# Performance work log

Hardware: AMD Instinct MI355X
Metric: run time of the kernel (lower is better)

## Reference

```python
import jax, jax.numpy as jnp
import numpy as np

NUM_EXPERTS = 32
TOP_K = 8
HIDDEN = 1536
INTER = 512


def setup_inputs() -> dict:
    key = jax.random.key(0)
    k1, k2, k3, k4 = jax.random.split(key, 4)
    hidden_states = jax.random.normal(k1, (4, 2048, HIDDEN), dtype=jnp.float32)
    # gate (router) weight: [E, H] as in nn.Linear(hidden, num_experts)
    gate_w = jax.random.normal(k2, (NUM_EXPERTS, HIDDEN), dtype=jnp.float32) * 0.02
    # fused gate+up projection per expert: [E, 2*I, H] (first I rows = gate/silu path)
    w13 = jax.random.normal(k3, (NUM_EXPERTS, 2 * INTER, HIDDEN), dtype=jnp.float32) * 0.02
    # down projection per expert: [E, H, I]
    w2 = jax.random.normal(k4, (NUM_EXPERTS, HIDDEN, INTER), dtype=jnp.float32) * 0.02
    return {"hidden_states": hidden_states, "gate_w": gate_w, "w13": w13, "w2": w2}


def _moe_forward(x, gate_w, w13, w2):
    orig_shape = x.shape
    x = x.reshape(-1, HIDDEN)            # [T, H]
    T = x.shape[0]

    # Router: softmax over all experts, then top-k, then renormalize.
    router_logits = x @ gate_w.T          # [T, E]
    probs = jax.nn.softmax(router_logits, axis=-1)
    topk_w, topk_idx = jax.lax.top_k(probs, TOP_K)        # [T, K]
    topk_w = topk_w / jnp.sum(topk_w, axis=-1, keepdims=True)

    # Scatter top-k weights into a dense [T, E] combine matrix (zeros elsewhere).
    expert_w = jnp.zeros((T, NUM_EXPERTS), dtype=x.dtype)
    expert_w = expert_w.at[jnp.arange(T)[:, None], topk_idx].add(topk_w)
    expert_w_eT = expert_w.T              # [E, T]

    def body(acc, ew):
        we, w13_e, w2_e = ew              # [T], [2I, H], [H, I]
        gu = x @ w13_e.T                  # [T, 2I]
        g, u = gu[:, :INTER], gu[:, INTER:]
        y = (jax.nn.silu(g) * u) @ w2_e.T  # [T, H]
        return acc + we[:, None] * y, None

    out, _ = jax.lax.scan(body, jnp.zeros_like(x), (expert_w_eT, w13, w2))
    return out.reshape(orig_shape)


def reference(hidden_states, gate_w, w13, w2):
    return _moe_forward(hidden_states, gate_w, w13, w2)
```

## Files before the change

### kernel.cpp

```cpp
#include <hip/hip_runtime.h>
#include <hip/hip_bf16.h>
#include <math.h>

#define NUM_EXPERTS 32
#define TOP_K 8
#define HIDDEN 1536
#define INTER 512

typedef __bf16 bf16_t;
typedef __bf16 bf16x8 __attribute__((ext_vector_type(8)));
typedef __bf16 bf16x4 __attribute__((ext_vector_type(4)));
typedef float f32x4 __attribute__((ext_vector_type(4)));

#define M_COUNTS    0
#define M_OFFSETS   32
#define M_CURSORS   96
#define M_NUMTILES  128
#define M_TILE_E    256
#define M_TILE_M0   1024
#define M_TILE_ROWS 2048
#define META_BYTES  16384

__device__ __forceinline__ void gld16(void* lds, const void* gsrc) {
  __builtin_amdgcn_global_load_lds(
      (const __attribute__((address_space(1))) void*)gsrc,
      (__attribute__((address_space(3))) void*)lds, 16, 0, 0);
}

__global__ __launch_bounds__(256) void k_cvt(
    const float* __restrict__ src, bf16_t* __restrict__ dst)
{
  size_t i = ((size_t)blockIdx.x * 256 + threadIdx.x) * 4;
  f32x4 v = *(const f32x4*)(src + i);
  bf16x4 o;
  o[0] = (bf16_t)v[0]; o[1] = (bf16_t)v[1]; o[2] = (bf16_t)v[2]; o[3] = (bf16_t)v[3];
  *(bf16x4*)(dst + i) = o;
}

__global__ __launch_bounds__(256) void k_tgw(
    const float* __restrict__ gw, float* __restrict__ gwT4)
{
  int tid = blockIdx.x * 256 + threadIdx.x;
  int e = tid / HIDDEN, k = tid % HIDDEN;
  gwT4[(k >> 2) * 128 + (e << 2) + (k & 3)] = gw[tid];
}

__global__ __launch_bounds__(64) void k_router(
    const float* __restrict__ x, const float* __restrict__ gwT4,
    int* __restrict__ meta, int* __restrict__ topk_idx, float* __restrict__ topk_w,
    bf16_t* __restrict__ x16)
{
  int t = blockIdx.x;
  int lane = threadIdx.x;
  int e = lane & 31, part = lane >> 5;
  const float* xrow = x + (size_t)t * HIDDEN;
  const f32x4* xr = (const f32x4*)(xrow + part * 768);
  const f32x4* gr = (const f32x4*)(gwT4 + part * 192 * 128 + e * 4);
  float s = 0.f;
#pragma unroll 4
  for (int i = 0; i < 192; ++i) {
    f32x4 xv = xr[i];
    f32x4 gv = gr[i * 32];
    s += xv[0] * gv[0] + xv[1] * gv[1] + xv[2] * gv[2] + xv[3] * gv[3];
  }
  s += __shfl_xor(s, 32);

  {
    const f32x4* xv4 = (const f32x4*)(xrow + lane * 24);
    bf16_t* xo = x16 + (size_t)t * HIDDEN + lane * 24;
#pragma unroll
    for (int i = 0; i < 6; ++i) {
      f32x4 v = xv4[i];
      bf16x4 o;
      o[0] = (bf16_t)v[0]; o[1] = (bf16_t)v[1]; o[2] = (bf16_t)v[2]; o[3] = (bf16_t)v[3];
      *(bf16x4*)(xo + i * 4) = o;
    }
  }

  float logit = s, rem = s;
  float m0 = 0.f, wsum = 0.f, my_l = 0.f;
  int my_e = 0;
#pragma unroll
  for (int k = 0; k < TOP_K; ++k) {
    float mx = rem;
#pragma unroll
    for (int off = 32; off >= 1; off >>= 1) mx = fmaxf(mx, __shfl_xor(mx, off));
    unsigned long long bal = __ballot(rem == mx);
    int src = __ffsll(bal) - 1;
    int ex = src & 31;
    float lv = __shfl(logit, ex);
    if (k == 0) m0 = mx;
    wsum += __expf(lv - m0);
    if (lane == k) { my_e = ex; my_l = lv; }
    if ((lane & 31) == ex) rem = -1e30f;
  }
  if (lane < TOP_K) {
    topk_idx[t * TOP_K + lane] = my_e;
    topk_w[t * TOP_K + lane] = __expf(my_l - m0) / wsum;
    atomicAdd(&meta[M_COUNTS + my_e], 1);
  }
}

__global__ void k_scan(int* __restrict__ meta)
{
  if (threadIdx.x != 0 || blockIdx.x != 0) return;
  int off = 0, nt = 0;
  for (int e = 0; e < NUM_EXPERTS; ++e) {
    int n = meta[M_COUNTS + e];
    meta[M_OFFSETS + e] = off;
    meta[M_CURSORS + e] = off;
    int tn = (n + 127) >> 7;
    for (int i = 0; i < tn; ++i) {
      meta[M_TILE_E + nt] = e;
      meta[M_TILE_M0 + nt] = off + i * 128;
      meta[M_TILE_ROWS + nt] = min(128, n - i * 128);
      ++nt;
    }
    off += n;
  }
  meta[M_OFFSETS + NUM_EXPERTS] = off;
  meta[M_NUMTILES] = nt;
}

__global__ __launch_bounds__(256) void k_scatter(
    const int* __restrict__ topk_idx,
    int* __restrict__ meta, int* __restrict__ pair_token, int* __restrict__ pair_pos)
{
  int i = blockIdx.x * 256 + threadIdx.x;
  int e = topk_idx[i];
  int pos = atomicAdd(&meta[M_CURSORS + e], 1);
  pair_token[pos] = i >> 3;
  pair_pos[i] = pos;
}

__global__ __launch_bounds__(256, 3) void k_gemm1(
    const bf16_t* __restrict__ x, const bf16_t* __restrict__ w13,
    const int* __restrict__ meta, const int* __restrict__ pair_token,
    bf16_t* __restrict__ act)
{
  int bid = blockIdx.x;
  int xcd = bid & 7, r2 = bid >> 3;
  int nb = r2 & 3, tile = xcd + 8 * (r2 >> 2);
  if (tile >= meta[M_NUMTILES]) return;
  int e    = meta[M_TILE_E + tile];
  int m0   = meta[M_TILE_M0 + tile];
  int rows = meta[M_TILE_ROWS + tile];
  int n0g  = nb * 128;

  __shared__ __align__(16) char smem[49152];
  char* As = smem;
  char* Bs = smem + 16384;

  int tid = threadIdx.x;
  int lane = tid & 63, w = tid >> 6;
  int cd = lane & 7;
  int lrow = w * 8 + (lane >> 3);

  const bf16_t* a_src[4];
  const bf16_t* b_src[8];
#pragma unroll
  for (int i = 0; i < 4; ++i) {
    int r = i * 32 + lrow;
    int rr = (r < rows) ? r : 0;
    int tok = pair_token[m0 + rr];
    int cg = cd ^ (r & 7);
    a_src[i] = x + (size_t)tok * HIDDEN + cg * 8;
  }
#pragma unroll
  for (int i = 0; i < 8; ++i) {
    int r = i * 32 + lrow;
    int cg = cd ^ (r & 7);
    int gr = (r < 128) ? (n0g + r) : (512 + n0g + (r - 128));
    b_src[i] = w13 + (size_t)e * (2 * INTER) * HIDDEN + (size_t)gr * HIDDEN + cg * 8;
  }
  unsigned lds_off = w * 1024 + lane * 16;

  f32x4 acc[2][16] = {};
  int q = lane >> 4, cl = lane & 15;
  int arow0 = (w * 32 + cl) * 128;
  int arow1 = (w * 32 + 16 + cl) * 128;

  for (int k0 = 0; k0 < HIDDEN; k0 += 64) {
#pragma unroll
    for (int i = 0; i < 4; ++i) gld16(As + i * 4096 + lds_off, a_src[i] + k0);
#pragma unroll
    for (int i = 0; i < 8; ++i) gld16(Bs + i * 4096 + lds_off, b_src[i] + k0);
    __syncthreads();
#pragma unroll
    for (int ks = 0; ks < 2; ++ks) {
      int csw = ((ks * 4 + q) ^ (lane & 7)) * 16;
      bf16x8 a0 = *(const bf16x8*)(As + arow0 + csw);
      bf16x8 a1 = *(const bf16x8*)(As + arow1 + csw);
#pragma unroll
      for (int in = 0; in < 16; ++in) {
        bf16x8 b = *(const bf16x8*)(Bs + (in * 16 + cl) * 128 + csw);
        acc[0][in] = __builtin_amdgcn_mfma_f32_16x16x32_bf16(a0, b, acc[0][in], 0, 0, 0);
        acc[1][in] = __builtin_amdgcn_mfma_f32_16x16x32_bf16(a1, b, acc[1][in], 0, 0, 0);
      }
    }
    __syncthreads();
  }

#pragma unroll
  for (int im = 0; im < 2; ++im) {
#pragma unroll
    for (int reg = 0; reg < 4; ++reg) {
      int row = w * 32 + im * 16 + q * 4 + reg;
      if (row < rows) {
        bf16_t* obase = act + (size_t)(m0 + row) * INTER + n0g + cl;
#pragma unroll
        for (int in = 0; in < 8; ++in) {
          float g = acc[im][in][reg];
          float u = acc[im][in + 8][reg];
          float a = (g / (1.f + __expf(-g))) * u;
          obase[in * 16] = (bf16_t)a;
        }
      }
    }
  }
}

__global__ __launch_bounds__(256, 3) void k_gemm2(
    const bf16_t* __restrict__ act, const bf16_t* __restrict__ w2,
    const int* __restrict__ meta, bf16_t* __restrict__ y, int n0base)
{
  int bid = blockIdx.x;
  int xcd = bid & 7, r2 = bid >> 3;
  int nb = r2 % 3, tile = xcd + 8 * (r2 / 3);
  if (tile >= meta[M_NUMTILES]) return;
  int e    = meta[M_TILE_E + tile];
  int m0   = meta[M_TILE_M0 + tile];
  int rows = meta[M_TILE_ROWS + tile];
  int n0l  = nb * 256;
  int n0   = n0base + n0l;

  __shared__ __align__(16) char smem[49152];
  char* As = smem;
  char* Bs = smem + 16384;

  int tid = threadIdx.x;
  int lane = tid & 63, w = tid >> 6;
  int cd = lane & 7;
  int lrow = w * 8 + (lane >> 3);

  const bf16_t* a_src[4];
  const bf16_t* b_src[8];
#pragma unroll
  for (int i = 0; i < 4; ++i) {
    int r = i * 32 + lrow;
    int rr = (r < rows) ? r : 0;
    int cg = cd ^ (r & 7);
    a_src[i] = act + (size_t)(m0 + rr) * INTER + cg * 8;
  }
#pragma unroll
  for (int i = 0; i < 8; ++i) {
    int r = i * 32 + lrow;
    int cg = cd ^ (r & 7);
    b_src[i] = w2 + (size_t)e * HIDDEN * INTER + (size_t)(n0 + r) * INTER + cg * 8;
  }
  unsigned lds_off = w * 1024 + lane * 16;

  f32x4 acc[2][16] = {};
  int q = lane >> 4, cl = lane & 15;
  int arow0 = (w * 32 + cl) * 128;
  int arow1 = (w * 32 + 16 + cl) * 128;

  for (int k0 = 0; k0 < INTER; k0 += 64) {
#pragma unroll
    for (int i = 0; i < 4; ++i) gld16(As + i * 4096 + lds_off, a_src[i] + k0);
#pragma unroll
    for (int i = 0; i < 8; ++i) gld16(Bs + i * 4096 + lds_off, b_src[i] + k0);
    __syncthreads();
#pragma unroll
    for (int ks = 0; ks < 2; ++ks) {
      int csw = ((ks * 4 + q) ^ (lane & 7)) * 16;
      bf16x8 a0 = *(const bf16x8*)(As + arow0 + csw);
      bf16x8 a1 = *(const bf16x8*)(As + arow1 + csw);
#pragma unroll
      for (int in = 0; in < 16; ++in) {
        bf16x8 b = *(const bf16x8*)(Bs + (in * 16 + cl) * 128 + csw);
        acc[0][in] = __builtin_amdgcn_mfma_f32_16x16x32_bf16(a0, b, acc[0][in], 0, 0, 0);
        acc[1][in] = __builtin_amdgcn_mfma_f32_16x16x32_bf16(a1, b, acc[1][in], 0, 0, 0);
      }
    }
    __syncthreads();
  }

#pragma unroll
  for (int im = 0; im < 2; ++im) {
#pragma unroll
    for (int reg = 0; reg < 4; ++reg) {
      int row = w * 32 + im * 16 + q * 4 + reg;
      if (row < rows) {
        bf16_t* obase = y + (size_t)(m0 + row) * 768 + n0l + cl;
#pragma unroll
        for (int in = 0; in < 16; ++in)
          obase[in * 16] = (bf16_t)acc[im][in][reg];
      }
    }
  }
}

__global__ __launch_bounds__(256) void k_combine(
    const bf16_t* __restrict__ y, const int* __restrict__ pair_pos,
    const float* __restrict__ topk_w, float* __restrict__ out, int colbase)
{
  int idx = blockIdx.x * 256 + threadIdx.x;
  int t = idx / 96, c = idx % 96;
  const int*   pp = pair_pos + t * 8;
  const float* tw = topk_w + t * 8;
  f32x4 sa = {}, sb = {};
#pragma unroll
  for (int k = 0; k < 8; ++k) {
    int pos = pp[k];
    float wgt = tw[k];
    bf16x8 v = *(const bf16x8*)(y + (size_t)pos * 768 + c * 8);
    sa[0] += wgt * (float)v[0]; sa[1] += wgt * (float)v[1];
    sa[2] += wgt * (float)v[2]; sa[3] += wgt * (float)v[3];
    sb[0] += wgt * (float)v[4]; sb[1] += wgt * (float)v[5];
    sb[2] += wgt * (float)v[6]; sb[3] += wgt * (float)v[7];
  }
  float* o = out + (size_t)t * HIDDEN + colbase + c * 8;
  *(f32x4*)o = sa;
  *(f32x4*)(o + 4) = sb;
}

extern "C" void kernel_launch(void* const* d_in, const int* in_sizes, int n_in,
                              void* d_out, int out_size, void* d_ws, size_t ws_size,
                              hipStream_t stream)
{
  const float* x   = (const float*)d_in[0];
  const float* gw  = (const float*)d_in[1];
  const float* w13 = (const float*)d_in[2];
  const float* w2  = (const float*)d_in[3];
  float* out = (float*)d_out;

  const int T = in_sizes[0] / HIDDEN;
  const int P = T * TOP_K;
  const size_t NX   = (size_t)T * HIDDEN;
  const size_t NW13 = (size_t)NUM_EXPERTS * 2 * INTER * HIDDEN;
  const size_t NW2  = (size_t)NUM_EXPERTS * HIDDEN * INTER;

  char* ws = (char*)d_ws;
  int*    meta        = (int*)ws;
  int*    topk_idx    = (int*)(ws + META_BYTES);
  float*  topk_w      = (float*)(ws + META_BYTES + (size_t)P * 4);
  int*    pair_token  = (int*)(ws + META_BYTES + (size_t)P * 8);
  int*    pair_pos    = (int*)(ws + META_BYTES + (size_t)P * 12);
  float*  gwT4        = (float*)(ws + (1536u << 10));
  size_t off = 2u << 20;
  bf16_t* w2_16  = (bf16_t*)(ws + off); off += NW2 * 2;
  bf16_t* act    = (bf16_t*)(ws + off); off += (size_t)P * INTER * 2;
  size_t y_off = off;
  bf16_t* x16    = (bf16_t*)(ws + off); off += NX * 2;
  bf16_t* w13_16 = (bf16_t*)(ws + off);
  bf16_t* y      = (bf16_t*)(ws + y_off);

  hipMemsetAsync(meta, 0, 32 * sizeof(int), stream);

  k_tgw<<<(HIDDEN * NUM_EXPERTS) / 256, 256, 0, stream>>>(gw, gwT4);
  k_cvt<<<NW13 / 1024, 256, 0, stream>>>(w13, w13_16);
  k_cvt<<<NW2 / 1024, 256, 0, stream>>>(w2, w2_16);

  k_router<<<T, 64, 0, stream>>>(x, gwT4, meta, topk_idx, topk_w, x16);
  k_scan<<<1, 64, 0, stream>>>(meta);
  k_scatter<<<P / 256, 256, 0, stream>>>(topk_idx, meta, pair_token, pair_pos);

  k_gemm1<<<544 * 4, 256, 0, stream>>>(x16, w13_16, meta, pair_token, act);

  k_gemm2<<<544 * 3, 256, 0, stream>>>(act, w2_16, meta, y, 0);
  k_combine<<<(T * 96) / 256, 256, 0, stream>>>(y, pair_pos, topk_w, out, 0);
  k_gemm2<<<544 * 3, 256, 0, stream>>>(act, w2_16, meta, y, 768);
  k_combine<<<(T * 96) / 256, 256, 0, stream>>>(y, pair_pos, topk_w, out, 768);
}
```

Measured before the change: 1.195 ms.

## Stage GEMM epilogues through LDS for vectorized stores and remap block-to-tile assignment

Both grouped GEMM kernels now write their output tile into a per-wave LDS staging buffer, then read it back and issue 16-byte vector stores of whole rows. Previously each lane wrote scattered 2-byte bf16 values. The block-to-work mapping is also changed so that each XCD gets a contiguous chunk of (tile, n-block) work items. This should improve L2 locality of expert weights per XCD. The cost is extra LDS traffic and no barrier between the LDS writes and reads, which relies on the LDS region being wave-private.

```diff
diff --git a/kernel.cpp b/kernel.cpp
--- a/kernel.cpp
+++ b/kernel.cpp
@@ -138,10 +138,13 @@
     const int* __restrict__ meta, const int* __restrict__ pair_token,
     bf16_t* __restrict__ act)
 {
-  int bid = blockIdx.x;
-  int xcd = bid & 7, r2 = bid >> 3;
-  int nb = r2 & 3, tile = xcd + 8 * (r2 >> 2);
-  if (tile >= meta[M_NUMTILES]) return;
+  int numtiles = meta[M_NUMTILES];
+  int xcd = blockIdx.x & 7, s = blockIdx.x >> 3;
+  int chunk = (numtiles * 4 + 7) >> 3;
+  if (s >= chunk) return;
+  int W = xcd * chunk + s;
+  int tile = W >> 2, nb = W & 3;
+  if (tile >= numtiles) return;
   int e    = meta[M_TILE_E + tile];
   int m0   = meta[M_TILE_M0 + tile];
   int rows = meta[M_TILE_ROWS + tile];
@@ -201,22 +204,28 @@
     __syncthreads();
   }
 
+  char* tb = smem + w * 8704;
 #pragma unroll
   for (int im = 0; im < 2; ++im) {
 #pragma unroll
     for (int reg = 0; reg < 4; ++reg) {
-      int row = w * 32 + im * 16 + q * 4 + reg;
-      if (row < rows) {
-        bf16_t* obase = act + (size_t)(m0 + row) * INTER + n0g + cl;
-#pragma unroll
-        for (int in = 0; in < 8; ++in) {
-          float g = acc[im][in][reg];
-          float u = acc[im][in + 8][reg];
-          float a = (g / (1.f + __expf(-g))) * u;
-          obase[in * 16] = (bf16_t)a;
-        }
+      int r = im * 16 + q * 4 + reg;
+#pragma unroll
+      for (int in = 0; in < 8; ++in) {
+        float g = acc[im][in][reg];
+        float u = acc[im][in + 8][reg];
+        float a = (g / (1.f + __expf(-g))) * u;
+        *(bf16_t*)(tb + r * 272 + (in * 16 + cl) * 2) = (bf16_t)a;
       }
     }
+  }
+#pragma unroll
+  for (int i = 0; i < 8; ++i) {
+    int r = (lane >> 4) + i * 4;
+    bf16x8 v = *(const bf16x8*)(tb + r * 272 + (lane & 15) * 16);
+    int row = w * 32 + r;
+    if (row < rows)
+      *(bf16x8*)(act + (size_t)(m0 + row) * INTER + n0g + (lane & 15) * 8) = v;
   }
 }
 
@@ -224,10 +233,13 @@
     const bf16_t* __restrict__ act, const bf16_t* __restrict__ w2,
     const int* __restrict__ meta, bf16_t* __restrict__ y, int n0base)
 {
-  int bid = blockIdx.x;
-  int xcd = bid & 7, r2 = bid >> 3;
-  int nb = r2 % 3, tile = xcd + 8 * (r2 / 3);
-  if (tile >= meta[M_NUMTILES]) return;
+  int numtiles = meta[M_NUMTILES];
+  int xcd = blockIdx.x & 7, s = blockIdx.x >> 3;
+  int chunk = (numtiles * 3 + 7) >> 3;
+  if (s >= chunk) return;
+  int W = xcd * chunk + s;
+  int tile = W / 3, nb = W - tile * 3;
+  if (tile >= numtiles) return;
   int e    = meta[M_TILE_E + tile];
   int m0   = meta[M_TILE_M0 + tile];
   int rows = meta[M_TILE_ROWS + tile];
@@ -286,17 +298,23 @@
     __syncthreads();
   }
 
+  char* tb = smem + w * 8448;
 #pragma unroll
   for (int im = 0; im < 2; ++im) {
 #pragma unroll
     for (int reg = 0; reg < 4; ++reg) {
-      int row = w * 32 + im * 16 + q * 4 + reg;
-      if (row < rows) {
-        bf16_t* obase = y + (size_t)(m0 + row) * 768 + n0l + cl;
-#pragma unroll
-        for (int in = 0; in < 16; ++in)
-          obase[in * 16] = (bf16_t)acc[im][in][reg];
-      }
+      int r = q * 4 + reg;
+#pragma unroll
+      for (int in = 0; in < 16; ++in)
+        *(bf16_t*)(tb + r * 528 + (in * 16 + cl) * 2) = (bf16_t)acc[im][in][reg];
+    }
+#pragma unroll
+    for (int i = 0; i < 8; ++i) {
+      int r = (lane >> 5) + i * 2;
+      bf16x8 v = *(const bf16x8*)(tb + r * 528 + (lane & 31) * 16);
+      int row = w * 32 + im * 16 + r;
+      if (row < rows)
+        *(bf16x8*)(y + (size_t)(m0 + row) * 768 + n0l + (lane & 31) * 8) = v;
     }
   }
 }
```

New measurement: 1.187 ms. No clear change (-0.7%).
